# Performance work log

Measured on AMD Instinct MI355X. Metric: run time of the kernel, lower is better.

The kernel has to match this reference:

```python
import jax, jax.numpy as jnp
import numpy as np

DIM = 1024
HEADS = 16
D_K = DIM // HEADS


def setup_inputs() -> dict:
    key = jax.random.key(0)
    k1, k2, k3, k4 = jax.random.split(key, 4)
    s = 1.0 / np.sqrt(DIM)
    return {
        "x": jax.random.normal(k1, (8, 1024, DIM), dtype=jnp.float32),
        "w_qkv": jax.random.uniform(k2, (DIM, 3 * DIM), dtype=jnp.float32, minval=-s, maxval=s),
        "w_out": jax.random.uniform(k3, (DIM, DIM), dtype=jnp.float32, minval=-s, maxval=s),
        "b_out": jax.random.uniform(k4, (DIM,), dtype=jnp.float32, minval=-s, maxval=s),
    }


def reference(x, w_qkv, w_out, b_out):
    B, N, _ = x.shape
    scale = D_K ** -0.5
    qkv = x @ w_qkv                                   # [B, N, 3*dim]
    q, k, v = jnp.split(qkv, 3, axis=-1)
    # [B, N, dim] -> [B, H, N, d_k]
    def heads(t):
        return t.reshape(B, N, HEADS, D_K).transpose(0, 2, 1, 3)
    q, k, v = heads(q), heads(k), heads(v)
    dots = jnp.einsum("bhnd,bhmd->bhnm", q, k) * scale  # [B, H, N, N]
    attn = jax.nn.softmax(dots, axis=-1)
    out = jnp.einsum("bhnm,bhmd->bhnd", attn, v)        # [B, H, N, d_k]
    out = out.transpose(0, 2, 1, 3).reshape(B, N, HEADS * D_K)
    return out @ w_out + b_out
```

## Files before the change

kernel.cpp:

```cpp
#include <hip/hip_runtime.h>
#include <hip/hip_bf16.h>
#include <math.h>


typedef __attribute__((ext_vector_type(8))) _Float16 f16x8;
typedef __attribute__((ext_vector_type(4))) _Float16 f16x4;
typedef __attribute__((ext_vector_type(4))) float f32x4;
typedef __attribute__((ext_vector_type(16))) float f32x16;
typedef __attribute__((ext_vector_type(4))) unsigned int u32x4;

#define QK_SCALE 0.18033688011112042f

#define GLOBAL_LOAD_LDS16(g, l) \
  __builtin_amdgcn_global_load_lds((const __attribute__((address_space(1))) void*)(g), \
                                   (__attribute__((address_space(3))) void*)(l), 16, 0, 0)

__global__ __launch_bounds__(256) void cast_f16(
    const float* __restrict__ in, _Float16* __restrict__ hi, int n4) {
  int i = blockIdx.x * blockDim.x + threadIdx.x;
  int stride = gridDim.x * blockDim.x;
  for (; i < n4; i += stride) {
    float4 v = ((const float4*)in)[i];
    f16x4 h;
    h[0] = (_Float16)v.x; h[1] = (_Float16)v.y;
    h[2] = (_Float16)v.z; h[3] = (_Float16)v.w;
    ((f16x4*)hi)[i] = h;
  }
}

__global__ __launch_bounds__(256) void cast_t_f16(
    const float* __restrict__ in, int R, int C, _Float16* __restrict__ hi) {
  __shared__ _Float16 hs[64][65];
  const int r0 = blockIdx.y * 64, c0 = blockIdx.x * 64;
  const int t = threadIdx.x;
#pragma unroll
  for (int it = 0; it < 4; ++it) {
    int r = (t >> 4) + it * 16;
    int cc = (t & 15) * 4;
    float4 v = *(const float4*)(in + (size_t)(r0 + r) * C + c0 + cc);
    hs[r][cc + 0] = (_Float16)v.x;
    hs[r][cc + 1] = (_Float16)v.y;
    hs[r][cc + 2] = (_Float16)v.z;
    hs[r][cc + 3] = (_Float16)v.w;
  }
  __syncthreads();
  const int oc = t >> 2;
  const int rr = (t & 3) * 16;
#pragma unroll
  for (int g = 0; g < 2; ++g) {
    f16x8 a;
#pragma unroll
    for (int j = 0; j < 8; ++j) a[j] = hs[rr + g * 8 + j][oc];
    *(f16x8*)(hi + (size_t)(c0 + oc) * R + r0 + rr + g * 8) = a;
  }
}

__global__ __launch_bounds__(256) void gemm1_qkv(
    const _Float16* __restrict__ Ah, const _Float16* __restrict__ Bh,
    _Float16* __restrict__ qkout, _Float16* __restrict__ vTout) {
  __shared__ char lds[34816];
  const int K = 1024;
  const int tid = threadIdx.x;
  const int wave = tid >> 6, lane = tid & 63;
  const int m0 = blockIdx.y * 128, n0 = blockIdx.x * 128;
  const int wr = wave >> 1, wc = wave & 1;

  const int srow = lane >> 2;
  const int sgchunk = (lane & 3) ^ ((srow >> 1) & 3);
  const int lr = lane & 15, kg = lane >> 4;
  const int rdoff = lr * 64 + ((kg ^ ((lr >> 1) & 3)) * 16);

  f32x4 acc[4][4];
#pragma unroll
  for (int m = 0; m < 4; ++m)
#pragma unroll
    for (int n = 0; n < 4; ++n) acc[m][n] = (f32x4){0.f, 0.f, 0.f, 0.f};

  const _Float16* gbase[2];
  gbase[0] = Ah + (size_t)m0 * K;
  gbase[1] = Bh + (size_t)n0 * K;

  for (int k0 = 0; k0 < K; k0 += 32) {
    __syncthreads();
#pragma unroll
    for (int p = 0; p < 2; ++p) {
#pragma unroll
      for (int half = 0; half < 2; ++half) {
        const int r16 = wave * 32 + half * 16;
        const _Float16* g = gbase[p] + (size_t)(r16 + srow) * K + k0 + sgchunk * 8;
        GLOBAL_LOAD_LDS16(g, lds + p * 8192 + r16 * 64);
      }
    }
    __syncthreads();

    f16x8 af[4], bf[4];
#pragma unroll
    for (int m = 0; m < 4; ++m)
      af[m] = *(const f16x8*)(lds + 0 * 8192 + (wr * 64 + m * 16) * 64 + rdoff);
#pragma unroll
    for (int n = 0; n < 4; ++n)
      bf[n] = *(const f16x8*)(lds + 1 * 8192 + (wc * 64 + n * 16) * 64 + rdoff);
#pragma unroll
    for (int m = 0; m < 4; ++m)
#pragma unroll
      for (int n = 0; n < 4; ++n)
        acc[m][n] = __builtin_amdgcn_mfma_f32_16x16x32_f16(af[m], bf[n], acc[m][n], 0, 0, 0);
  }

  const int crow = (lane >> 4) * 4, ccol = lane & 15;
  if (n0 < 2048) {
    const float qsc = (n0 < 1024) ? (float)QK_SCALE : 1.0f;
#pragma unroll
    for (int m = 0; m < 4; ++m) {
#pragma unroll
      for (int n = 0; n < 4; ++n) {
        const int rbase = m0 + wr * 64 + m * 16 + crow;
        const int c = n0 + wc * 64 + n * 16 + ccol;
#pragma unroll
        for (int i = 0; i < 4; ++i)
          qkout[(size_t)(rbase + i) * 2048 + c] = (_Float16)(acc[m][n][i] * qsc);
      }
    }
  } else {
    __syncthreads();
    _Float16* lv = (_Float16*)lds;
#pragma unroll
    for (int m = 0; m < 4; ++m)
#pragma unroll
      for (int n = 0; n < 4; ++n) {
        const int cc = wc * 64 + n * 16 + ccol;
#pragma unroll
        for (int i = 0; i < 4; ++i) {
          const int r = wr * 64 + m * 16 + crow + i;
          lv[cc * 136 + r] = (_Float16)acc[m][n][i];
        }
      }
    __syncthreads();
    const int bb = m0 >> 10, seq0 = m0 & 1023;
    const int hbase = (n0 - 2048) >> 6;
#pragma unroll
    for (int it = 0; it < 8; ++it) {
      const int idx = tid + it * 256;
      const int cc = idx >> 4, ch = idx & 15;
      f16x8 v = *(const f16x8*)(lv + cc * 136 + ch * 8);
      const int hh = hbase + (cc >> 6), d = cc & 63;
      *(f16x8*)(vTout + (((size_t)bb * 16 + hh) * 64 + d) * 1024 + seq0 + ch * 8) = v;
    }
  }
}

__global__ __launch_bounds__(256) void attn_mfma(
    const _Float16* __restrict__ qk,
    const _Float16* __restrict__ vT,
    _Float16* __restrict__ ao) {
  const int hb   = blockIdx.x;
  const int h    = hb >> 3;
  const int b    = hb & 7;
  const int band = blockIdx.y;
  const int tid  = threadIdx.x;
  const int wave = tid >> 6;
  const int lane = tid & 63;
  const int l31  = lane & 31;
  const int hi   = lane >> 5;
  const int kswz = (l31 & 7) << 4;

  __shared__ _Float16 Ks[2][64 * 64];
  __shared__ _Float16 Vt[2][64 * 64];

  const _Float16* vbase = vT + ((size_t)(b * 16 + h) * 64) * 1024;

  const int qrow_g = b * 1024 + band * 128 + wave * 32 + l31;
  f16x8 qf[4];
#pragma unroll
  for (int c = 0; c < 4; ++c)
    qf[c] = *(const f16x8*)(qk + (size_t)qrow_g * 2048 + h * 64 + c * 16 + hi * 8);

  f16x8 vones;
#pragma unroll
  for (int j = 0; j < 8; ++j) vones[j] = (_Float16)1.0f;

  f32x16 accO0 = {0}, accO1 = {0}, accL = {0};

  f16x8 kr[2], vr[2];
  const int sr = tid >> 3, sc8 = tid & 7;

  auto load_t = [&](int t) {
#pragma unroll
    for (int it = 0; it < 2; ++it) {
      const int r = sr + it * 32;
      kr[it] = *(const f16x8*)(qk + (size_t)(b * 1024 + t * 64 + r) * 2048 +
                               1024 + h * 64 + sc8 * 8);
      vr[it] = *(const f16x8*)(vbase + (size_t)r * 1024 + t * 64 + sc8 * 8);
    }
  };
  auto write_buf = [&](int buf) {
#pragma unroll
    for (int it = 0; it < 2; ++it) {
      const int r = sr + it * 32;
      const int off = r * 128 + ((sc8 * 16) ^ ((r & 7) << 4));
      *(f16x8*)((char*)&Ks[buf][0] + off) = kr[it];
      *(f16x8*)((char*)&Vt[buf][0] + off) = vr[it];
    }
  };

  load_t(0);
  write_buf(0);

  for (int t = 0; t < 16; ++t) {
    __syncthreads();
    if (t < 15) load_t(t + 1);
    const int buf = t & 1;
    const char* ksb = (const char*)&Ks[buf][0];
    const char* vtb = (const char*)&Vt[buf][0];

    f32x16 accS0 = {0}, accS1 = {0};
    __builtin_amdgcn_s_setprio(1);
#pragma unroll
    for (int c = 0; c < 4; ++c) {
      f16x8 ka0 = *(const f16x8*)(ksb + l31 * 128 + ((c * 32 + hi * 16) ^ kswz));
      f16x8 ka1 = *(const f16x8*)(ksb + (l31 + 32) * 128 + ((c * 32 + hi * 16) ^ kswz));
      accS0 = __builtin_amdgcn_mfma_f32_32x32x16_f16(ka0, qf[c], accS0, 0, 0, 0);
      accS1 = __builtin_amdgcn_mfma_f32_32x32x16_f16(ka1, qf[c], accS1, 0, 0, 0);
    }
    __builtin_amdgcn_s_setprio(0);

#pragma unroll
    for (int c = 0; c < 4; ++c) {
      float e[8];
#pragma unroll
      for (int k = 0; k < 8; ++k)
        e[k] = __builtin_exp2f((c < 2) ? accS0[(c & 1) * 8 + k]
                                       : accS1[(c & 1) * 8 + k]);
      unsigned q0a = __builtin_bit_cast(unsigned, __builtin_amdgcn_cvt_pkrtz(e[0], e[1]));
      unsigned q0b = __builtin_bit_cast(unsigned, __builtin_amdgcn_cvt_pkrtz(e[2], e[3]));
      unsigned q1a = __builtin_bit_cast(unsigned, __builtin_amdgcn_cvt_pkrtz(e[4], e[5]));
      unsigned q1b = __builtin_bit_cast(unsigned, __builtin_amdgcn_cvt_pkrtz(e[6], e[7]));
      unsigned send_a = hi ? q0a : q1a;
      unsigned send_b = hi ? q0b : q1b;
      unsigned recv_a = __shfl_xor(send_a, 32);
      unsigned recv_b = __shfl_xor(send_b, 32);
      u32x4 pu;
      pu[0] = hi ? recv_a : q0a;
      pu[1] = hi ? recv_b : q0b;
      pu[2] = hi ? q1a : recv_a;
      pu[3] = hi ? q1b : recv_b;
      f16x8 pa = __builtin_bit_cast(f16x8, pu);

      const int kchunk = ((2 * c + hi) * 16) ^ kswz;
      f16x8 vb0 = *(const f16x8*)(vtb + l31 * 128 + kchunk);
      f16x8 vb1 = *(const f16x8*)(vtb + (l31 + 32) * 128 + kchunk);
      __builtin_amdgcn_s_setprio(1);
      accO0 = __builtin_amdgcn_mfma_f32_32x32x16_f16(pa, vb0, accO0, 0, 0, 0);
      accO1 = __builtin_amdgcn_mfma_f32_32x32x16_f16(pa, vb1, accO1, 0, 0, 0);
      accL  = __builtin_amdgcn_mfma_f32_32x32x16_f16(pa, vones, accL, 0, 0, 0);
      __builtin_amdgcn_s_setprio(0);
    }

    if (t < 15) write_buf((t + 1) & 1);
  }

#pragma unroll
  for (int reg = 0; reg < 16; ++reg) {
    const int qr = (reg & 3) + 8 * (reg >> 2) + 4 * hi;
    const float il = 1.f / accL[reg];
    const size_t grow = (size_t)(b * 1024 + band * 128 + wave * 32 + qr) * 1024 + h * 64;
    ao[grow + l31]      = (_Float16)(accO0[reg] * il);
    ao[grow + 32 + l31] = (_Float16)(accO1[reg] * il);
  }
}

__global__ __launch_bounds__(256) void gemm2_out(
    const _Float16* __restrict__ A,
    const _Float16* __restrict__ B,
    float* __restrict__ C, const float* __restrict__ bias) {
  __shared__ char lds[2 * 8192];
  const int K = 1024;
  const int tid = threadIdx.x;
  const int wave = tid >> 6, lane = tid & 63;
  const int m0 = blockIdx.y * 128, n0 = blockIdx.x * 128;
  const int wr = wave >> 1, wc = wave & 1;

  const int srow = lane >> 2;
  const int sgchunk = (lane & 3) ^ ((srow >> 1) & 3);
  const int lr = lane & 15, kg = lane >> 4;
  const int rdoff = lr * 64 + ((kg ^ ((lr >> 1) & 3)) * 16);

  f32x4 acc[4][4];
#pragma unroll
  for (int m = 0; m < 4; ++m)
#pragma unroll
    for (int n = 0; n < 4; ++n) acc[m][n] = (f32x4){0.f, 0.f, 0.f, 0.f};

  const _Float16* gbase[2];
  gbase[0] = A + (size_t)m0 * K;
  gbase[1] = B + (size_t)n0 * K;

  for (int k0 = 0; k0 < K; k0 += 32) {
    __syncthreads();
#pragma unroll
    for (int p = 0; p < 2; ++p) {
#pragma unroll
      for (int half = 0; half < 2; ++half) {
        const int r16 = wave * 32 + half * 16;
        const _Float16* g = gbase[p] + (size_t)(r16 + srow) * K + k0 + sgchunk * 8;
        GLOBAL_LOAD_LDS16(g, lds + p * 8192 + r16 * 64);
      }
    }
    __syncthreads();

    f16x8 af[4], bf[4];
#pragma unroll
    for (int m = 0; m < 4; ++m)
      af[m] = *(const f16x8*)(lds + 0 * 8192 + (wr * 64 + m * 16) * 64 + rdoff);
#pragma unroll
    for (int n = 0; n < 4; ++n)
      bf[n] = *(const f16x8*)(lds + 1 * 8192 + (wc * 64 + n * 16) * 64 + rdoff);
#pragma unroll
    for (int m = 0; m < 4; ++m)
#pragma unroll
      for (int n = 0; n < 4; ++n)
        acc[m][n] = __builtin_amdgcn_mfma_f32_16x16x32_f16(af[m], bf[n], acc[m][n], 0, 0, 0);
  }

  const int crow = (lane >> 4) * 4, ccol = lane & 15;
#pragma unroll
  for (int m = 0; m < 4; ++m) {
#pragma unroll
    for (int n = 0; n < 4; ++n) {
      const int rbase = m0 + wr * 64 + m * 16 + crow;
      const int c = n0 + wc * 64 + n * 16 + ccol;
      const float bv = bias[c];
#pragma unroll
      for (int i = 0; i < 4; ++i)
        C[(size_t)(rbase + i) * 1024 + c] = acc[m][n][i] + bv;
    }
  }
}

extern "C" void kernel_launch(void* const* d_in, const int* in_sizes, int n_in,
                              void* d_out, int out_size, void* d_ws, size_t ws_size,
                              hipStream_t stream) {
  const float* x     = (const float*)d_in[0];
  const float* w_qkv = (const float*)d_in[1];
  const float* w_out = (const float*)d_in[2];
  const float* b_out = (const float*)d_in[3];
  float* out = (float*)d_out;

  char* ws = (char*)d_ws;
  _Float16* xh  = (_Float16*)(ws);
  _Float16* ao  = xh;
  _Float16* wqT = (_Float16*)(ws + (32u << 20));
  _Float16* woT = (_Float16*)(ws + (44u << 20));
  _Float16* qkp = (_Float16*)(ws + (48u << 20));
  _Float16* vT  = (_Float16*)(ws + (80u << 20));

  cast_f16<<<2048, 256, 0, stream>>>(x, xh, 8192 * 1024 / 4);
  cast_t_f16<<<dim3(48, 16), 256, 0, stream>>>(w_qkv, 1024, 3072, wqT);
  cast_t_f16<<<dim3(16, 16), 256, 0, stream>>>(w_out, 1024, 1024, woT);

  gemm1_qkv<<<dim3(24, 64), 256, 0, stream>>>(xh, wqT, qkp, vT);

  attn_mfma<<<dim3(128, 8), 256, 0, stream>>>(qkp, vT, ao);

  gemm2_out<<<dim3(8, 64), 256, 0, stream>>>(ao, woT, out, b_out);
}
```

Measured before the change: 180.1 us.

## Process 64 query rows per wave in attention to reuse K/V tiles

Each wave in the attention kernel now handles two 32-row query sub-tiles instead of one, so every block covers 256 query rows and the grid is halved. K fragments are read from LDS once per tile and reused for both sub-tiles, and each V fragment feeds two output accumulators. This halves K/V global and LDS traffic per query row and improves the MFMA-to-load ratio. In exchange it roughly doubles accumulator and Q register use, which may reduce occupancy, and halves the number of blocks (512) available to fill the CUs.

```diff
diff --git a/kernel.cpp b/kernel.cpp
--- a/kernel.cpp
+++ b/kernel.cpp
@@ -169,17 +169,20 @@
 
   const _Float16* vbase = vT + ((size_t)(b * 16 + h) * 64) * 1024;
 
-  const int qrow_g = b * 1024 + band * 128 + wave * 32 + l31;
-  f16x8 qf[4];
-#pragma unroll
-  for (int c = 0; c < 4; ++c)
-    qf[c] = *(const f16x8*)(qk + (size_t)qrow_g * 2048 + h * 64 + c * 16 + hi * 8);
+  const int row0 = b * 1024 + band * 256 + wave * 64;
+  f16x8 qf0[4], qf1[4];
+#pragma unroll
+  for (int c = 0; c < 4; ++c) {
+    qf0[c] = *(const f16x8*)(qk + (size_t)(row0 + l31) * 2048 + h * 64 + c * 16 + hi * 8);
+    qf1[c] = *(const f16x8*)(qk + (size_t)(row0 + 32 + l31) * 2048 + h * 64 + c * 16 + hi * 8);
+  }
 
   f16x8 vones;
 #pragma unroll
   for (int j = 0; j < 8; ++j) vones[j] = (_Float16)1.0f;
 
-  f32x16 accO0 = {0}, accO1 = {0}, accL = {0};
+  f32x16 accO00 = {0}, accO01 = {0}, accO10 = {0}, accO11 = {0};
+  f32x16 accL0 = {0}, accL1 = {0};
 
   f16x8 kr[2], vr[2];
   const int sr = tid >> 3, sc8 = tid & 7;
@@ -213,46 +216,64 @@
     const char* ksb = (const char*)&Ks[buf][0];
     const char* vtb = (const char*)&Vt[buf][0];
 
-    f32x16 accS0 = {0}, accS1 = {0};
-    __builtin_amdgcn_s_setprio(1);
+    f16x8 ka0[4], ka1[4];
 #pragma unroll
     for (int c = 0; c < 4; ++c) {
-      f16x8 ka0 = *(const f16x8*)(ksb + l31 * 128 + ((c * 32 + hi * 16) ^ kswz));
-      f16x8 ka1 = *(const f16x8*)(ksb + (l31 + 32) * 128 + ((c * 32 + hi * 16) ^ kswz));
-      accS0 = __builtin_amdgcn_mfma_f32_32x32x16_f16(ka0, qf[c], accS0, 0, 0, 0);
-      accS1 = __builtin_amdgcn_mfma_f32_32x32x16_f16(ka1, qf[c], accS1, 0, 0, 0);
-    }
-    __builtin_amdgcn_s_setprio(0);
+      ka0[c] = *(const f16x8*)(ksb + l31 * 128 + ((c * 32 + hi * 16) ^ kswz));
+      ka1[c] = *(const f16x8*)(ksb + (l31 + 32) * 128 + ((c * 32 + hi * 16) ^ kswz));
+    }
+
+    u32x4 pa0[4], pa1[4];
+#pragma unroll
+    for (int set = 0; set < 2; ++set) {
+      f32x16 accS0 = {0}, accS1 = {0};
+      __builtin_amdgcn_s_setprio(1);
+#pragma unroll
+      for (int c = 0; c < 4; ++c) {
+        f16x8 q = set ? qf1[c] : qf0[c];
+        accS0 = __builtin_amdgcn_mfma_f32_32x32x16_f16(ka0[c], q, accS0, 0, 0, 0);
+        accS1 = __builtin_amdgcn_mfma_f32_32x32x16_f16(ka1[c], q, accS1, 0, 0, 0);
+      }
+      __builtin_amdgcn_s_setprio(0);
+
+#pragma unroll
+      for (int c = 0; c < 4; ++c) {
+        float e[8];
+#pragma unroll
+        for (int k = 0; k < 8; ++k)
+          e[k] = __builtin_exp2f((c < 2) ? accS0[(c & 1) * 8 + k]
+                                         : accS1[(c & 1) * 8 + k]);
+        unsigned q0a = __builtin_bit_cast(unsigned, __builtin_amdgcn_cvt_pkrtz(e[0], e[1]));
+        unsigned q0b = __builtin_bit_cast(unsigned, __builtin_amdgcn_cvt_pkrtz(e[2], e[3]));
+        unsigned q1a = __builtin_bit_cast(unsigned, __builtin_amdgcn_cvt_pkrtz(e[4], e[5]));
+        unsigned q1b = __builtin_bit_cast(unsigned, __builtin_amdgcn_cvt_pkrtz(e[6], e[7]));
+        unsigned send_a = hi ? q0a : q1a;
+        unsigned send_b = hi ? q0b : q1b;
+        unsigned recv_a = __shfl_xor(send_a, 32);
+        unsigned recv_b = __shfl_xor(send_b, 32);
+        u32x4 pu;
+        pu[0] = hi ? recv_a : q0a;
+        pu[1] = hi ? recv_b : q0b;
+        pu[2] = hi ? q1a : recv_a;
+        pu[3] = hi ? q1b : recv_b;
+        if (set) pa1[c] = pu; else pa0[c] = pu;
+      }
+    }
 
 #pragma unroll
     for (int c = 0; c < 4; ++c) {
-      float e[8];
-#pragma unroll
-      for (int k = 0; k < 8; ++k)
-        e[k] = __builtin_exp2f((c < 2) ? accS0[(c & 1) * 8 + k]
-                                       : accS1[(c & 1) * 8 + k]);
-      unsigned q0a = __builtin_bit_cast(unsigned, __builtin_amdgcn_cvt_pkrtz(e[0], e[1]));
-      unsigned q0b = __builtin_bit_cast(unsigned, __builtin_amdgcn_cvt_pkrtz(e[2], e[3]));
-      unsigned q1a = __builtin_bit_cast(unsigned, __builtin_amdgcn_cvt_pkrtz(e[4], e[5]));
-      unsigned q1b = __builtin_bit_cast(unsigned, __builtin_amdgcn_cvt_pkrtz(e[6], e[7]));
-      unsigned send_a = hi ? q0a : q1a;
-      unsigned send_b = hi ? q0b : q1b;
-      unsigned recv_a = __shfl_xor(send_a, 32);
-      unsigned recv_b = __shfl_xor(send_b, 32);
-      u32x4 pu;
-      pu[0] = hi ? recv_a : q0a;
-      pu[1] = hi ? recv_b : q0b;
-      pu[2] = hi ? q1a : recv_a;
-      pu[3] = hi ? q1b : recv_b;
-      f16x8 pa = __builtin_bit_cast(f16x8, pu);
-
       const int kchunk = ((2 * c + hi) * 16) ^ kswz;
       f16x8 vb0 = *(const f16x8*)(vtb + l31 * 128 + kchunk);
       f16x8 vb1 = *(const f16x8*)(vtb + (l31 + 32) * 128 + kchunk);
+      f16x8 p0 = __builtin_bit_cast(f16x8, pa0[c]);
+      f16x8 p1 = __builtin_bit_cast(f16x8, pa1[c]);
       __builtin_amdgcn_s_setprio(1);
-      accO0 = __builtin_amdgcn_mfma_f32_32x32x16_f16(pa, vb0, accO0, 0, 0, 0);
-      accO1 = __builtin_amdgcn_mfma_f32_32x32x16_f16(pa, vb1, accO1, 0, 0, 0);
-      accL  = __builtin_amdgcn_mfma_f32_32x32x16_f16(pa, vones, accL, 0, 0, 0);
+      accO00 = __builtin_amdgcn_mfma_f32_32x32x16_f16(p0, vb0, accO00, 0, 0, 0);
+      accO01 = __builtin_amdgcn_mfma_f32_32x32x16_f16(p0, vb1, accO01, 0, 0, 0);
+      accO10 = __builtin_amdgcn_mfma_f32_32x32x16_f16(p1, vb0, accO10, 0, 0, 0);
+      accO11 = __builtin_amdgcn_mfma_f32_32x32x16_f16(p1, vb1, accO11, 0, 0, 0);
+      accL0  = __builtin_amdgcn_mfma_f32_32x32x16_f16(p0, vones, accL0, 0, 0, 0);
+      accL1  = __builtin_amdgcn_mfma_f32_32x32x16_f16(p1, vones, accL1, 0, 0, 0);
       __builtin_amdgcn_s_setprio(0);
     }
 
@@ -262,10 +283,18 @@
 #pragma unroll
   for (int reg = 0; reg < 16; ++reg) {
     const int qr = (reg & 3) + 8 * (reg >> 2) + 4 * hi;
-    const float il = 1.f / accL[reg];
-    const size_t grow = (size_t)(b * 1024 + band * 128 + wave * 32 + qr) * 1024 + h * 64;
-    ao[grow + l31]      = (_Float16)(accO0[reg] * il);
-    ao[grow + 32 + l31] = (_Float16)(accO1[reg] * il);
+    {
+      const float il = 1.f / accL0[reg];
+      const size_t grow = (size_t)(row0 + qr) * 1024 + h * 64;
+      ao[grow + l31]      = (_Float16)(accO00[reg] * il);
+      ao[grow + 32 + l31] = (_Float16)(accO01[reg] * il);
+    }
+    {
+      const float il = 1.f / accL1[reg];
+      const size_t grow = (size_t)(row0 + 32 + qr) * 1024 + h * 64;
+      ao[grow + l31]      = (_Float16)(accO10[reg] * il);
+      ao[grow + 32 + l31] = (_Float16)(accO11[reg] * il);
+    }
   }
 }
 
@@ -360,7 +389,7 @@
 
   gemm1_qkv<<<dim3(24, 64), 256, 0, stream>>>(xh, wqT, qkp, vT);
 
-  attn_mfma<<<dim3(128, 8), 256, 0, stream>>>(qkp, vT, ao);
+  attn_mfma<<<dim3(128, 4), 256, 0, stream>>>(qkp, vT, ao);
 
   gemm2_out<<<dim3(8, 64), 256, 0, stream>>>(ao, woT, out, b_out);
 }
```

Measured after the change: 199.7 us. +10.9%, slower.
